# Kernel optimization log

Measured on AMD Instinct MI355X. Metric: run time of the kernel, lower is better.

## Reference

```python
import jax, jax.numpy as jnp
import numpy as np


def setup_inputs() -> dict:
    key = jax.random.key(0)
    ks = jax.random.split(key, 7)
    B, D, N, R = 256, 5120, 16, 160  # batch, d_inner, d_state, dt_rank
    x = jax.random.normal(ks[0], (B, D), jnp.float32)
    h0 = jax.random.normal(ks[1], (B, D, N), jnp.float32)
    W_x_dt = jax.random.normal(ks[2], (D, R), jnp.float32) * (1.0 / np.sqrt(D))
    W_dt = jax.random.normal(ks[3], (R, D), jnp.float32) * (1.0 / np.sqrt(R))
    b_dt = jax.random.normal(ks[4], (D,), jnp.float32)
    W_BC = jax.random.normal(ks[5], (D, 2 * N), jnp.float32) * (1.0 / np.sqrt(D))
    A_log = jax.random.normal(ks[6], (D, N), jnp.float32)
    return {"x": x, "h0": h0, "W_x_dt": W_x_dt, "W_dt": W_dt,
            "b_dt": b_dt, "W_BC": W_BC, "A_log": A_log}


def reference(x, h0, W_x_dt, W_dt, b_dt, W_BC, A_log):
    # Single-token Mamba selective SSM step (batch dims squeezed: x [B,D], h0 [B,D,N]).
    N = A_log.shape[1]
    # delta_t = softplus(dt_proj(delta_t_proj(x)))  -> [B, D]
    dt = jax.nn.softplus((x @ W_x_dt) @ W_dt + b_dt)
    # BC projection, split into B and C parts -> [B, N] each
    BC = x @ W_BC
    Bm, Cm = BC[:, :N], BC[:, N:]
    A = -jnp.exp(A_log)                              # [D, N]
    delta_A = jnp.exp(A[None, :, :] * dt[:, :, None])   # [B, D, N]
    delta_Bx = (dt * x)[:, :, None] * Bm[:, None, :]     # [B, D, N]
    h = delta_A * h0 + delta_Bx                          # new hidden state
    # y = h @ C (per-batch bmm over state dim) + x residual
    y = jnp.einsum('bdn,bn->bd', h, Cm) + x              # [B, D]
    return y
```

## Files before the change

kernel.cpp:

```cpp
#include <hip/hip_runtime.h>
#include <math.h>

#define BB 256
#define DD 5120
#define NN 16
#define RR 160
#define CT 192
#define NSPLIT 32
#define TMP_ELEMS (BB * CT)
#define NEGA_ELEMS (DD * NN)

__global__ __launch_bounds__(256) void k1_gemm(const float* __restrict__ x,
                                               const float* __restrict__ Wxdt,
                                               const float* __restrict__ Wbc,
                                               float* __restrict__ part) {
    __shared__ float xs[32][68];
    __shared__ float ws[32][64];
    const int tid = threadIdx.x;
    const int tx = tid & 15, ty = tid >> 4;
    const int c0 = blockIdx.x * 64;
    const int b0 = blockIdx.y * 64;
    const int k0 = blockIdx.z * 160;
    float acc[4][4] = {};

    for (int kc = 0; kc < 160; kc += 32) {
        {
            const int i  = tid >> 3;
            const int j4 = (tid & 7) * 4;
            #pragma unroll
            for (int rep = 0; rep < 2; ++rep) {
                const int row = i + rep * 32;
                const float4 v = *(const float4*)&x[(size_t)(b0 + row) * DD + k0 + kc + j4];
                xs[j4 + 0][row] = v.x;
                xs[j4 + 1][row] = v.y;
                xs[j4 + 2][row] = v.z;
                xs[j4 + 3][row] = v.w;
            }
        }
        {
            const int c4 = (tid & 15) * 4;
            const int r0 = tid >> 4;
            #pragma unroll
            for (int rep = 0; rep < 2; ++rep) {
                const int r  = r0 + rep * 16;
                const int kg = k0 + kc + r;
                const int cg = c0 + c4;
                float4 v;
                if (cg < RR) v = *(const float4*)&Wxdt[(size_t)kg * RR + cg];
                else         v = *(const float4*)&Wbc[(size_t)kg * 32 + (cg - RR)];
                *(float4*)&ws[r][c4] = v;
            }
        }
        __syncthreads();
        #pragma unroll
        for (int k = 0; k < 32; ++k) {
            const float4 a4 = *(const float4*)&xs[k][ty * 4];
            const float4 w4 = *(const float4*)&ws[k][tx * 4];
            const float av[4] = {a4.x, a4.y, a4.z, a4.w};
            const float wv[4] = {w4.x, w4.y, w4.z, w4.w};
            #pragma unroll
            for (int u = 0; u < 4; ++u)
                #pragma unroll
                for (int v = 0; v < 4; ++v)
                    acc[u][v] = fmaf(av[u], wv[v], acc[u][v]);
        }
        __syncthreads();
    }

    float* p = part + (size_t)blockIdx.z * TMP_ELEMS;
    #pragma unroll
    for (int u = 0; u < 4; ++u) {
        const int b = b0 + ty * 4 + u;
        *(float4*)&p[b * CT + c0 + tx * 4] =
            make_float4(acc[u][0], acc[u][1], acc[u][2], acc[u][3]);
    }
}

__global__ __launch_bounds__(256) void k_red(const float* __restrict__ part,
                                             const float* __restrict__ Alog,
                                             float* __restrict__ tmp,
                                             float* __restrict__ negA) {
    const int idx = blockIdx.x * 256 + threadIdx.x;
    if (idx < TMP_ELEMS) {
        float s = 0.f;
        #pragma unroll
        for (int z = 0; z < NSPLIT; ++z) s += part[(size_t)z * TMP_ELEMS + idx];
        tmp[idx] = s;
    } else {
        const int j = idx - TMP_ELEMS;
        negA[j] = -__expf(Alog[j]);
    }
}

__global__ __launch_bounds__(256) void k_fused(const float* __restrict__ x,
                                               const float* __restrict__ h0,
                                               const float* __restrict__ Wdt,
                                               const float* __restrict__ bdt,
                                               const float* __restrict__ tmp,
                                               const float* __restrict__ negA,
                                               float* __restrict__ out) {
    __shared__ float ts[4][CT];
    const int tid = threadIdx.x;
    const int b0 = blockIdx.x * 4;
    const int d  = blockIdx.y * 256 + tid;

    for (int p = tid; p < 4 * CT; p += 256)
        ts[p / CT][p % CT] = tmp[(size_t)b0 * CT + p];
    __syncthreads();

    const float* wcol = Wdt + d;
    float acc[4] = {0.f, 0.f, 0.f, 0.f};
    #pragma unroll 2
    for (int k8 = 0; k8 < RR; k8 += 8) {
        float w[8];
        #pragma unroll
        for (int j = 0; j < 8; ++j) w[j] = wcol[(size_t)(k8 + j) * DD];
        #pragma unroll
        for (int bi = 0; bi < 4; ++bi) {
            const float* tr = &ts[bi][k8];
            #pragma unroll
            for (int j = 0; j < 8; ++j)
                acc[bi] = fmaf(tr[j], w[j], acc[bi]);
        }
    }

    float av[16];
    {
        const float* ap = &negA[(size_t)d * NN];
        #pragma unroll
        for (int n4 = 0; n4 < NN; n4 += 4) {
            const float4 a4 = *(const float4*)&ap[n4];
            av[n4 + 0] = a4.x; av[n4 + 1] = a4.y;
            av[n4 + 2] = a4.z; av[n4 + 3] = a4.w;
        }
    }
    const float bdv = bdt[d];

    #pragma unroll
    for (int bi = 0; bi < 4; ++bi) {
        const float z  = acc[bi] + bdv;
        const float dt = fmaxf(z, 0.f) + log1pf(__expf(-fabsf(z)));
        const size_t cell = (size_t)(b0 + bi) * DD + d;
        const float xe  = x[cell];
        const float dtx = dt * xe;
        const float* hp = &h0[cell * NN];
        const float* bm = &ts[bi][RR];
        const float* cm = &ts[bi][RR + 16];
        float acc4[4] = {xe, 0.f, 0.f, 0.f};
        #pragma unroll
        for (int n4 = 0; n4 < NN; n4 += 4) {
            const float4 h4 = *(const float4*)&hp[n4];
            const float hv[4] = {h4.x, h4.y, h4.z, h4.w};
            #pragma unroll
            for (int q = 0; q < 4; ++q) {
                const int n = n4 + q;
                const float dA = __expf(av[n] * dt);
                const float h  = fmaf(dA, hv[q], dtx * bm[n]);
                acc4[q] = fmaf(h, cm[n], acc4[q]);
            }
        }
        out[cell] = (acc4[0] + acc4[1]) + (acc4[2] + acc4[3]);
    }
}

extern "C" void kernel_launch(void* const* d_in, const int* in_sizes, int n_in,
                              void* d_out, int out_size, void* d_ws, size_t ws_size,
                              hipStream_t stream) {
    const float* x    = (const float*)d_in[0];
    const float* h0   = (const float*)d_in[1];
    const float* Wxdt = (const float*)d_in[2];
    const float* Wdt  = (const float*)d_in[3];
    const float* bdt  = (const float*)d_in[4];
    const float* Wbc  = (const float*)d_in[5];
    const float* Alog = (const float*)d_in[6];
    float* out = (float*)d_out;

    float* part = (float*)d_ws;
    float* tmp  = part + (size_t)NSPLIT * TMP_ELEMS;
    float* negA = tmp + TMP_ELEMS;

    k1_gemm<<<dim3(3, 4, NSPLIT), 256, 0, stream>>>(x, Wxdt, Wbc, part);
    k_red<<<dim3((TMP_ELEMS + NEGA_ELEMS) / 256), 256, 0, stream>>>(part, Alog, tmp, negA);
    k_fused<<<dim3(BB / 4, DD / 256), 256, 0, stream>>>(x, h0, Wdt, bdt, tmp, negA, out);
}
```

Before: 175.7 us.

## Widen GEMM split-K, halve fused-kernel batch tile, prefetch h0 before dt GEMV

The first GEMM now splits K into 160 chunks of 32 instead of 32 chunks of 160, removing its inner K loop and launching many more blocks. The reduction kernel therefore sums 160 partials per element instead of 32. The fused kernel handles 2 batch rows per block instead of 4, doubling the grid, and issues the h0 and x loads before the Wdt GEMV so the large h0 stream overlaps the GEMV compute. The tradeoffs are 5x more partial-sum traffic to write and reduce, and Wdt reread by twice as many blocks.

```diff
diff --git a/kernel.cpp b/kernel.cpp
--- a/kernel.cpp
+++ b/kernel.cpp
@@ -6,7 +6,8 @@
 #define NN 16
 #define RR 160
 #define CT 192
-#define NSPLIT 32
+#define NSPLIT 160
+#define KSPLIT 32
 #define TMP_ELEMS (BB * CT)
 #define NEGA_ELEMS (DD * NN)
 
@@ -20,51 +21,49 @@
     const int tx = tid & 15, ty = tid >> 4;
     const int c0 = blockIdx.x * 64;
     const int b0 = blockIdx.y * 64;
-    const int k0 = blockIdx.z * 160;
+    const int k0 = blockIdx.z * KSPLIT;
+
+    {
+        const int i  = tid >> 3;
+        const int j4 = (tid & 7) * 4;
+        #pragma unroll
+        for (int rep = 0; rep < 2; ++rep) {
+            const int row = i + rep * 32;
+            const float4 v = *(const float4*)&x[(size_t)(b0 + row) * DD + k0 + j4];
+            xs[j4 + 0][row] = v.x;
+            xs[j4 + 1][row] = v.y;
+            xs[j4 + 2][row] = v.z;
+            xs[j4 + 3][row] = v.w;
+        }
+    }
+    {
+        const int c4 = (tid & 15) * 4;
+        const int r0 = tid >> 4;
+        #pragma unroll
+        for (int rep = 0; rep < 2; ++rep) {
+            const int r  = r0 + rep * 16;
+            const int kg = k0 + r;
+            const int cg = c0 + c4;
+            float4 v;
+            if (cg < RR) v = *(const float4*)&Wxdt[(size_t)kg * RR + cg];
+            else         v = *(const float4*)&Wbc[(size_t)kg * 32 + (cg - RR)];
+            *(float4*)&ws[r][c4] = v;
+        }
+    }
+    __syncthreads();
+
     float acc[4][4] = {};
-
-    for (int kc = 0; kc < 160; kc += 32) {
-        {
-            const int i  = tid >> 3;
-            const int j4 = (tid & 7) * 4;
+    #pragma unroll
+    for (int k = 0; k < KSPLIT; ++k) {
+        const float4 a4 = *(const float4*)&xs[k][ty * 4];
+        const float4 w4 = *(const float4*)&ws[k][tx * 4];
+        const float av[4] = {a4.x, a4.y, a4.z, a4.w};
+        const float wv[4] = {w4.x, w4.y, w4.z, w4.w};
+        #pragma unroll
+        for (int u = 0; u < 4; ++u)
             #pragma unroll
-            for (int rep = 0; rep < 2; ++rep) {
-                const int row = i + rep * 32;
-                const float4 v = *(const float4*)&x[(size_t)(b0 + row) * DD + k0 + kc + j4];
-                xs[j4 + 0][row] = v.x;
-                xs[j4 + 1][row] = v.y;
-                xs[j4 + 2][row] = v.z;
-                xs[j4 + 3][row] = v.w;
-            }
-        }
-        {
-            const int c4 = (tid & 15) * 4;
-            const int r0 = tid >> 4;
-            #pragma unroll
-            for (int rep = 0; rep < 2; ++rep) {
-                const int r  = r0 + rep * 16;
-                const int kg = k0 + kc + r;
-                const int cg = c0 + c4;
-                float4 v;
-                if (cg < RR) v = *(const float4*)&Wxdt[(size_t)kg * RR + cg];
-                else         v = *(const float4*)&Wbc[(size_t)kg * 32 + (cg - RR)];
-                *(float4*)&ws[r][c4] = v;
-            }
-        }
-        __syncthreads();
-        #pragma unroll
-        for (int k = 0; k < 32; ++k) {
-            const float4 a4 = *(const float4*)&xs[k][ty * 4];
-            const float4 w4 = *(const float4*)&ws[k][tx * 4];
-            const float av[4] = {a4.x, a4.y, a4.z, a4.w};
-            const float wv[4] = {w4.x, w4.y, w4.z, w4.w};
-            #pragma unroll
-            for (int u = 0; u < 4; ++u)
-                #pragma unroll
-                for (int v = 0; v < 4; ++v)
-                    acc[u][v] = fmaf(av[u], wv[v], acc[u][v]);
-        }
-        __syncthreads();
+            for (int v = 0; v < 4; ++v)
+                acc[u][v] = fmaf(av[u], wv[v], acc[u][v]);
     }
 
     float* p = part + (size_t)blockIdx.z * TMP_ELEMS;
@@ -83,7 +82,7 @@
     const int idx = blockIdx.x * 256 + threadIdx.x;
     if (idx < TMP_ELEMS) {
         float s = 0.f;
-        #pragma unroll
+        #pragma unroll 8
         for (int z = 0; z < NSPLIT; ++z) s += part[(size_t)z * TMP_ELEMS + idx];
         tmp[idx] = s;
     } else {
@@ -99,24 +98,35 @@
                                                const float* __restrict__ tmp,
                                                const float* __restrict__ negA,
                                                float* __restrict__ out) {
-    __shared__ float ts[4][CT];
+    __shared__ float ts[2][CT];
     const int tid = threadIdx.x;
-    const int b0 = blockIdx.x * 4;
+    const int b0 = blockIdx.x * 2;
     const int d  = blockIdx.y * 256 + tid;
 
-    for (int p = tid; p < 4 * CT; p += 256)
+    for (int p = tid; p < 2 * CT; p += 256)
         ts[p / CT][p % CT] = tmp[(size_t)b0 * CT + p];
     __syncthreads();
 
+    float4 h4[2][4];
+    float  xe[2];
+    #pragma unroll
+    for (int bi = 0; bi < 2; ++bi) {
+        const size_t cell = (size_t)(b0 + bi) * DD + d;
+        xe[bi] = x[cell];
+        const float* hp = &h0[cell * NN];
+        #pragma unroll
+        for (int j = 0; j < 4; ++j) h4[bi][j] = *(const float4*)&hp[j * 4];
+    }
+
     const float* wcol = Wdt + d;
-    float acc[4] = {0.f, 0.f, 0.f, 0.f};
+    float acc[2] = {0.f, 0.f};
     #pragma unroll 2
     for (int k8 = 0; k8 < RR; k8 += 8) {
         float w[8];
         #pragma unroll
         for (int j = 0; j < 8; ++j) w[j] = wcol[(size_t)(k8 + j) * DD];
         #pragma unroll
-        for (int bi = 0; bi < 4; ++bi) {
+        for (int bi = 0; bi < 2; ++bi) {
             const float* tr = &ts[bi][k8];
             #pragma unroll
             for (int j = 0; j < 8; ++j)
@@ -137,23 +147,20 @@
     const float bdv = bdt[d];
 
     #pragma unroll
-    for (int bi = 0; bi < 4; ++bi) {
+    for (int bi = 0; bi < 2; ++bi) {
         const float z  = acc[bi] + bdv;
         const float dt = fmaxf(z, 0.f) + log1pf(__expf(-fabsf(z)));
         const size_t cell = (size_t)(b0 + bi) * DD + d;
-        const float xe  = x[cell];
-        const float dtx = dt * xe;
-        const float* hp = &h0[cell * NN];
+        const float dtx = dt * xe[bi];
         const float* bm = &ts[bi][RR];
         const float* cm = &ts[bi][RR + 16];
-        float acc4[4] = {xe, 0.f, 0.f, 0.f};
+        float acc4[4] = {xe[bi], 0.f, 0.f, 0.f};
         #pragma unroll
-        for (int n4 = 0; n4 < NN; n4 += 4) {
-            const float4 h4 = *(const float4*)&hp[n4];
-            const float hv[4] = {h4.x, h4.y, h4.z, h4.w};
+        for (int j = 0; j < 4; ++j) {
+            const float hv[4] = {h4[bi][j].x, h4[bi][j].y, h4[bi][j].z, h4[bi][j].w};
             #pragma unroll
             for (int q = 0; q < 4; ++q) {
-                const int n = n4 + q;
+                const int n = j * 4 + q;
                 const float dA = __expf(av[n] * dt);
                 const float h  = fmaf(dA, hv[q], dtx * bm[n]);
                 acc4[q] = fmaf(h, cm[n], acc4[q]);
@@ -181,5 +188,5 @@
 
     k1_gemm<<<dim3(3, 4, NSPLIT), 256, 0, stream>>>(x, Wxdt, Wbc, part);
     k_red<<<dim3((TMP_ELEMS + NEGA_ELEMS) / 256), 256, 0, stream>>>(part, Alog, tmp, negA);
-    k_fused<<<dim3(BB / 4, DD / 256), 256, 0, stream>>>(x, h0, Wdt, bdt, tmp, negA, out);
+    k_fused<<<dim3(BB / 2, DD / 256), 256, 0, stream>>>(x, h0, Wdt, bdt, tmp, negA, out);
 }
```

New measurement: 189.4 us. 7.8% more time.

## Split dt projection into tiled split-K GEMM and separate SSM epilogue kernel

Applied to the files above, without the earlier changes.

Replaces the fused kernel, where each thread ran a skinny 4-row dot product over W_dt, with a register-tiled 64x64 split-K GEMM (k_dt) that writes four partial dt planes. A new epilogue kernel sums those partials, then assigns four lanes per (b,d) cell to share the 16 state elements and reduces across them with warp shuffles. The aim is better reuse of W_dt and more parallelism with coalesced h0 reads. The cost is an extra launch and about 21 MB of partial-dt traffic written and read back through global memory.

```diff
diff --git a/kernel.cpp b/kernel.cpp
--- a/kernel.cpp
+++ b/kernel.cpp
@@ -7,6 +7,7 @@
 #define RR 160
 #define CT 192
 #define NSPLIT 32
+#define DTSPLIT 4
 #define TMP_ELEMS (BB * CT)
 #define NEGA_ELEMS (DD * NN)
 
@@ -92,74 +93,100 @@
     }
 }
 
-__global__ __launch_bounds__(256) void k_fused(const float* __restrict__ x,
-                                               const float* __restrict__ h0,
-                                               const float* __restrict__ Wdt,
-                                               const float* __restrict__ bdt,
-                                               const float* __restrict__ tmp,
-                                               const float* __restrict__ negA,
-                                               float* __restrict__ out) {
-    __shared__ float ts[4][CT];
+__global__ __launch_bounds__(256) void k_dt(const float* __restrict__ tmp,
+                                            const float* __restrict__ Wdt,
+                                            float* __restrict__ dtp) {
+    __shared__ float ts[40][68];
+    __shared__ float ws[40][64];
     const int tid = threadIdx.x;
-    const int b0 = blockIdx.x * 4;
-    const int d  = blockIdx.y * 256 + tid;
-
-    for (int p = tid; p < 4 * CT; p += 256)
-        ts[p / CT][p % CT] = tmp[(size_t)b0 * CT + p];
+    const int tx = tid & 15, ty = tid >> 4;
+    const int d0 = blockIdx.x * 64;
+    const int b0 = blockIdx.y * 64;
+    const int k0 = blockIdx.z * 40;
+
+    for (int p = tid; p < 640; p += 256) {
+        const int row = p / 10;
+        const int j4  = (p % 10) * 4;
+        const float4 v = *(const float4*)&tmp[(size_t)(b0 + row) * CT + k0 + j4];
+        ts[j4 + 0][row] = v.x; ts[j4 + 1][row] = v.y;
+        ts[j4 + 2][row] = v.z; ts[j4 + 3][row] = v.w;
+    }
+    for (int p = tid; p < 640; p += 256) {
+        const int r  = p >> 4;
+        const int c4 = (p & 15) * 4;
+        *(float4*)&ws[r][c4] = *(const float4*)&Wdt[(size_t)(k0 + r) * DD + d0 + c4];
+    }
     __syncthreads();
 
-    const float* wcol = Wdt + d;
-    float acc[4] = {0.f, 0.f, 0.f, 0.f};
+    float acc[4][4] = {};
+    #pragma unroll 8
+    for (int k = 0; k < 40; ++k) {
+        const float4 a4 = *(const float4*)&ts[k][ty * 4];
+        const float4 w4 = *(const float4*)&ws[k][tx * 4];
+        const float av[4] = {a4.x, a4.y, a4.z, a4.w};
+        const float wv[4] = {w4.x, w4.y, w4.z, w4.w};
+        #pragma unroll
+        for (int u = 0; u < 4; ++u)
+            #pragma unroll
+            for (int v = 0; v < 4; ++v)
+                acc[u][v] = fmaf(av[u], wv[v], acc[u][v]);
+    }
+
+    float* p = dtp + (size_t)blockIdx.z * BB * DD;
+    #pragma unroll
+    for (int u = 0; u < 4; ++u) {
+        const int b = b0 + ty * 4 + u;
+        *(float4*)&p[(size_t)b * DD + d0 + tx * 4] =
+            make_float4(acc[u][0], acc[u][1], acc[u][2], acc[u][3]);
+    }
+}
+
+__global__ __launch_bounds__(256) void k_epi(const float* __restrict__ x,
+                                             const float* __restrict__ h0,
+                                             const float* __restrict__ dtp,
+                                             const float* __restrict__ bdt,
+                                             const float* __restrict__ tmp,
+                                             const float* __restrict__ negA,
+                                             float* __restrict__ out) {
+    __shared__ float bc[32];
+    const int tid = threadIdx.x;
+    const int b     = blockIdx.y;
+    const int dbase = blockIdx.x * 512;
+    if (tid < 32) bc[tid] = tmp[(size_t)b * CT + RR + tid];
+    __syncthreads();
+
+    const int g = tid >> 2;
+    const int q = tid & 3;
+    const float4 bm4 = *(const float4*)&bc[q * 4];
+    const float4 cm4 = *(const float4*)&bc[16 + q * 4];
+
     #pragma unroll 2
-    for (int k8 = 0; k8 < RR; k8 += 8) {
-        float w[8];
-        #pragma unroll
-        for (int j = 0; j < 8; ++j) w[j] = wcol[(size_t)(k8 + j) * DD];
-        #pragma unroll
-        for (int bi = 0; bi < 4; ++bi) {
-            const float* tr = &ts[bi][k8];
-            #pragma unroll
-            for (int j = 0; j < 8; ++j)
-                acc[bi] = fmaf(tr[j], w[j], acc[bi]);
-        }
-    }
-
-    float av[16];
-    {
-        const float* ap = &negA[(size_t)d * NN];
-        #pragma unroll
-        for (int n4 = 0; n4 < NN; n4 += 4) {
-            const float4 a4 = *(const float4*)&ap[n4];
-            av[n4 + 0] = a4.x; av[n4 + 1] = a4.y;
-            av[n4 + 2] = a4.z; av[n4 + 3] = a4.w;
-        }
-    }
-    const float bdv = bdt[d];
-
-    #pragma unroll
-    for (int bi = 0; bi < 4; ++bi) {
-        const float z  = acc[bi] + bdv;
+    for (int cc = 0; cc < 8; ++cc) {
+        const int d = dbase + cc * 64 + g;
+        const size_t cell = (size_t)b * DD + d;
+
+        float ps = dtp[(size_t)q * BB * DD + cell];
+        ps += __shfl_xor(ps, 1);
+        ps += __shfl_xor(ps, 2);
+        const float z  = ps + bdt[d];
         const float dt = fmaxf(z, 0.f) + log1pf(__expf(-fabsf(z)));
-        const size_t cell = (size_t)(b0 + bi) * DD + d;
+
         const float xe  = x[cell];
         const float dtx = dt * xe;
-        const float* hp = &h0[cell * NN];
-        const float* bm = &ts[bi][RR];
-        const float* cm = &ts[bi][RR + 16];
-        float acc4[4] = {xe, 0.f, 0.f, 0.f};
-        #pragma unroll
-        for (int n4 = 0; n4 < NN; n4 += 4) {
-            const float4 h4 = *(const float4*)&hp[n4];
-            const float hv[4] = {h4.x, h4.y, h4.z, h4.w};
-            #pragma unroll
-            for (int q = 0; q < 4; ++q) {
-                const int n = n4 + q;
-                const float dA = __expf(av[n] * dt);
-                const float h  = fmaf(dA, hv[q], dtx * bm[n]);
-                acc4[q] = fmaf(h, cm[n], acc4[q]);
-            }
-        }
-        out[cell] = (acc4[0] + acc4[1]) + (acc4[2] + acc4[3]);
+        const float4 an = *(const float4*)&negA[(size_t)d * NN + q * 4];
+        const float4 hv = *(const float4*)&h0[cell * NN + q * 4];
+
+        float r;
+        {
+            const float h0v = fmaf(__expf(an.x * dt), hv.x, dtx * bm4.x);
+            const float h1v = fmaf(__expf(an.y * dt), hv.y, dtx * bm4.y);
+            const float h2v = fmaf(__expf(an.z * dt), hv.z, dtx * bm4.z);
+            const float h3v = fmaf(__expf(an.w * dt), hv.w, dtx * bm4.w);
+            r = (h0v * cm4.x + h1v * cm4.y) + (h2v * cm4.z + h3v * cm4.w);
+        }
+        r += __shfl_xor(r, 1);
+        r += __shfl_xor(r, 2);
+        if (q == 0) out[cell] = r + xe;
     }
 }
 
@@ -178,8 +205,10 @@
     float* part = (float*)d_ws;
     float* tmp  = part + (size_t)NSPLIT * TMP_ELEMS;
     float* negA = tmp + TMP_ELEMS;
+    float* dtp  = negA + NEGA_ELEMS;
 
     k1_gemm<<<dim3(3, 4, NSPLIT), 256, 0, stream>>>(x, Wxdt, Wbc, part);
     k_red<<<dim3((TMP_ELEMS + NEGA_ELEMS) / 256), 256, 0, stream>>>(part, Alog, tmp, negA);
-    k_fused<<<dim3(BB / 4, DD / 256), 256, 0, stream>>>(x, h0, Wdt, bdt, tmp, negA, out);
-}
+    k_dt<<<dim3(DD / 64, BB / 64, DTSPLIT), 256, 0, stream>>>(tmp, Wdt, dtp);
+    k_epi<<<dim3(DD / 512, BB), 256, 0, stream>>>(x, h0, dtp, bdt, tmp, negA, out);
+}
```

Result: slower. 179.9 us (+2.4%).
